# Optimization experiments

Measured on AMD Instinct MI355X. Metric: run time of the kernel, lower is better.

Reference implementation:

```python
import jax, jax.numpy as jnp
import numpy as np

N_TAU = 10      # hardcoded in source (dt = tau / N_tau)
N_STEPS = 500   # N = floor(T/dt) with T=50, tau=1.0 -> dt=0.1
B, D, H = 1024, 128, 512


def setup_inputs() -> dict:
    key = jax.random.key(0)
    k0, k1, k2 = jax.random.split(key, 3)
    return {
        "x0": jax.random.normal(k0, (B, D), dtype=jnp.float32),
        "tau": jnp.ones((1,), dtype=jnp.float32),
        "W1": jax.random.normal(k1, (H, 2 * D + 1), dtype=jnp.float32) * (2 * D + 1) ** -0.5,
        "b1": jnp.zeros((H,), dtype=jnp.float32),
        "W2": jax.random.normal(k2, (D, H), dtype=jnp.float32) * H ** -0.5,
        "b2": jnp.zeros((D,), dtype=jnp.float32),
    }


def reference(x0, tau, W1, b1, W2, b2):
    """Forward-Euler DDE solve: x'(t) = F(x(t), x(t-tau), t), x(t)=x0 for t<=0.
    F(x, y, t) = W2 @ tanh(W1 @ [x; y; t] + b1) + b2, batched over B trajectories.
    Returns the trajectory with shape [N_STEPS+1, B, D]."""
    dt = tau[0] / N_TAU

    def F(x, y, t):
        # x, y: [B, D]; t: traced scalar
        tcol = jnp.full((x.shape[0], 1), 1.0, x.dtype) * t
        z = jnp.concatenate([x, y, tcol], axis=-1)          # [B, 2D+1]
        h = jnp.tanh(z @ W1.T + b1)                          # [B, H]
        return h @ W2.T + b2                                 # [B, D]

    # delay buffer: buf[0] = x_{n-N_tau} (delayed state), buf[-1] = x_n (current)
    buf0 = jnp.broadcast_to(x0, (N_TAU + 1,) + x0.shape)     # constant history X0

    def step(buf, n):
        t = n.astype(x0.dtype) * dt
        x_new = buf[-1] + dt * F(buf[-1], buf[0], t)
        buf = jnp.concatenate([buf[1:], x_new[None]], axis=0)
        return buf, x_new

    _, xs = jax.lax.scan(step, buf0, jnp.arange(N_STEPS))
    return jnp.concatenate([x0[None], xs], axis=0)           # [N+1, B, D]
```

## Files before the change

### kernel.cpp

```cpp
#include <hip/hip_runtime.h>

typedef float f32x4 __attribute__((ext_vector_type(4)));
typedef _Float16 f16x8 __attribute__((ext_vector_type(8)));

#define B_TOT   1024
#define D_DIM   128
#define H_DIM   512
#define N_STEPS 500
#define ROWS    4
#define WAVES   8

#define HSTRIDE 272
#define HSLOT   (8 * HSTRIDE)
#define BSTRIDE 1056
#define LDS_BOUNCE (11 * HSLOT)
#define LDS_TOTAL  (LDS_BOUNCE + 8 * BSTRIDE)

static __device__ __forceinline__ short f16b(float f) {
    _Float16 h = (_Float16)f;
    return __builtin_bit_cast(short, h);
}
static __device__ __forceinline__ float f16tof(short s) {
    return (float)__builtin_bit_cast(_Float16, s);
}
static __device__ __forceinline__ float tanh_fast(float x) {
    float e = __builtin_amdgcn_exp2f(x * 2.885390081777927f);
    return 1.0f - 2.0f * __builtin_amdgcn_rcpf(e + 1.0f);
}
static __device__ __forceinline__ f32x4 sx32(f32x4 v) {
    f32x4 r;
#pragma unroll
    for (int i = 0; i < 4; ++i) r[i] = __shfl_xor(v[i], 32);
    return r;
}
static __device__ __forceinline__ float pick(f32x4 v, int g) {
    float lo = (g & 1) ? v[1] : v[0];
    float hi = (g & 1) ? v[3] : v[2];
    return (g & 2) ? hi : lo;
}

__global__ __launch_bounds__(512, 2) void ndde_kernel(
    const float* __restrict__ x0, const float* __restrict__ tau,
    const float* __restrict__ W1, const float* __restrict__ b1,
    const float* __restrict__ W2, const float* __restrict__ b2,
    float* __restrict__ out)
{
    __shared__ __align__(16) char smem[LDS_TOTAL];

    const int tid = threadIdx.x;
    const int w   = tid >> 6;
    const int l   = tid & 63;
    const int g   = l >> 4;
    const int l15 = l & 15;
    const int ur  = (l15 & 3) | ((l15 >> 3) << 2);
    const int r0  = blockIdx.x * ROWS;
    const int d   = 16 * w + l15;

    const float dtv = tau[0] * 0.1f;

    f16x8 w1f[4][8];
    f16x8 w2f[16];
    float b1f[4], w1tf[4];

#pragma unroll
    for (int nt = 0; nt < 4; ++nt) {
        const int hr = 64 * w + 16 * nt + l15;
        const float* wr = W1 + (long)hr * 257;
#pragma unroll
        for (int ks = 0; ks < 8; ++ks) {
            const int c0 = 32 * ks + 8 * g;
            f16x8 f;
#pragma unroll
            for (int j = 0; j < 8; ++j) f[j] = (_Float16)wr[c0 + j];
            w1f[nt][ks] = f;
        }
        b1f[nt]  = b1[hr];
        w1tf[nt] = wr[256];
    }
    {
        const float* wr = W2 + (long)d * 512;
#pragma unroll
        for (int ks = 0; ks < 16; ++ks) {
            const int c0 = 32 * ks + 8 * g;
            f16x8 f;
#pragma unroll
            for (int j = 0; j < 8; ++j) f[j] = (_Float16)wr[c0 + j];
            w2f[ks] = f;
        }
    }
    const float b2v = b2[d];
    float xo = x0[(long)(r0 + g) * D_DIM + d];

    {
        short hb = f16b(xo);
        short lb = f16b(xo - f16tof(hb));
        for (int s = 0; s < 11; ++s) {
            *(short*)(smem + s * HSLOT + g * HSTRIDE + 2 * d)       = hb;
            *(short*)(smem + s * HSLOT + (g + 4) * HSTRIDE + 2 * d) = lb;
        }
        out[(long)(r0 + g) * D_DIM + d] = xo;
    }
    __syncthreads();

    const int histRd   = ur * HSTRIDE + 16 * g;
    const int bounceRd = LDS_BOUNCE + ur * BSTRIDE + ((16 * g) ^ ((ur & 3) << 4));
    const int bwXor    = g << 4;

    float* po = out + (long)(B_TOT * D_DIM) + (long)(r0 + g) * D_DIM + d;

    int cur = 0;
    int ys  = 1;

#pragma clang loop unroll(disable)
    for (int n = 0; n < N_STEPS; ++n) {
        const float t = (float)n * dtv;

        f32x4 acc1[4];
#pragma unroll
        for (int nt = 0; nt < 4; ++nt) acc1[nt] = (f32x4){0.f, 0.f, 0.f, 0.f};

        const char* xb = smem + cur * HSLOT + histRd;
        const char* yb = smem + ys * HSLOT + histRd;
#pragma unroll
        for (int ks = 0; ks < 4; ++ks) {
            f16x8 xa = *(const f16x8*)(xb + 64 * ks);
#pragma unroll
            for (int nt = 0; nt < 4; ++nt)
                acc1[nt] = __builtin_amdgcn_mfma_f32_16x16x32_f16(xa, w1f[nt][ks], acc1[nt], 0, 0, 0);
        }
#pragma unroll
        for (int ks = 0; ks < 4; ++ks) {
            f16x8 ya = *(const f16x8*)(yb + 64 * ks);
#pragma unroll
            for (int nt = 0; nt < 4; ++nt)
                acc1[nt] = __builtin_amdgcn_mfma_f32_16x16x32_f16(ya, w1f[nt][ks + 4], acc1[nt], 0, 0, 0);
        }

#pragma unroll
        for (int nt = 0; nt < 4; ++nt) {
            f32x4 c = acc1[nt];
            c += sx32(c);
            float hp = pick(c, g) + fmaf(t, w1tf[nt], b1f[nt]);
            float h  = tanh_fast(hp);
            short hh = f16b(h);
            short hl = f16b(h - f16tof(hh));
            const int cb = (2 * (64 * w + 16 * nt + l15)) ^ bwXor;
            *(short*)(smem + LDS_BOUNCE + g * BSTRIDE + cb)       = hh;
            *(short*)(smem + LDS_BOUNCE + (g + 4) * BSTRIDE + cb) = hl;
        }
        __syncthreads();

        f32x4 acc2 = (f32x4){0.f, 0.f, 0.f, 0.f};
#pragma unroll
        for (int ks = 0; ks < 16; ++ks) {
            f16x8 ha = *(const f16x8*)(smem + bounceRd + 64 * ks);
            acc2 = __builtin_amdgcn_mfma_f32_16x16x32_f16(ha, w2f[ks], acc2, 0, 0, 0);
        }
        acc2 += sx32(acc2);

        const float o  = pick(acc2, g) + b2v;
        const float xn = fmaf(dtv, o, xo);
        xo = xn;
        {
            short hb = f16b(xn);
            short lb = f16b(xn - f16tof(hb));
            *(short*)(smem + ys * HSLOT + g * HSTRIDE + 2 * d)       = hb;
            *(short*)(smem + ys * HSLOT + (g + 4) * HSTRIDE + 2 * d) = lb;
        }
        *po = xn;
        po += B_TOT * D_DIM;

        cur = ys;
        ys  = ys + 1;
        if (ys == 11) ys = 0;
        __syncthreads();
    }
}

extern "C" void kernel_launch(void* const* d_in, const int* in_sizes, int n_in,
                              void* d_out, int out_size, void* d_ws, size_t ws_size,
                              hipStream_t stream) {
    (void)in_sizes; (void)n_in; (void)out_size; (void)d_ws; (void)ws_size;
    const float* x0  = (const float*)d_in[0];
    const float* tau = (const float*)d_in[1];
    const float* W1  = (const float*)d_in[2];
    const float* b1  = (const float*)d_in[3];
    const float* W2  = (const float*)d_in[4];
    const float* b2  = (const float*)d_in[5];
    float* out = (float*)d_out;

    ndde_kernel<<<dim3(B_TOT / ROWS), dim3(64 * WAVES), 0, stream>>>(
        x0, tau, W1, b1, W2, b2, out);
}
```

Before: 948.1 us.

## Keep layer-2 inputs in registers, split W2 by hidden slice, reduce partials across waves

Each wave now computes the first layer transposed (weights as the A operand), so the tanh activations stay in registers as the B operand of second-layer MFMAs over that wave's own 64-row hidden slice. Partial D outputs are written to an LDS slab and summed across the 8 waves by a scalar reduction. This removes the activation bounce through LDS. The bias and time term are folded into an extra small MFMA, and the half-wave reduction now uses a DPP lane swap instead of shuffles. In exchange it issues twice as many second-layer MFMAs (hi and lo parts of the activation) and adds an 8-way cross-wave LDS reduction.

```diff
diff --git a/kernel.cpp b/kernel.cpp
--- a/kernel.cpp
+++ b/kernel.cpp
@@ -2,41 +2,31 @@
 
 typedef float f32x4 __attribute__((ext_vector_type(4)));
 typedef _Float16 f16x8 __attribute__((ext_vector_type(8)));
+typedef _Float16 f16x4 __attribute__((ext_vector_type(4)));
+typedef int i32x4 __attribute__((ext_vector_type(4)));
+typedef int i32x2 __attribute__((ext_vector_type(2)));
 
 #define B_TOT   1024
 #define D_DIM   128
-#define H_DIM   512
 #define N_STEPS 500
 #define ROWS    4
 #define WAVES   8
 
 #define HSTRIDE 272
 #define HSLOT   (8 * HSTRIDE)
-#define BSTRIDE 1056
-#define LDS_BOUNCE (11 * HSLOT)
-#define LDS_TOTAL  (LDS_BOUNCE + 8 * BSTRIDE)
-
-static __device__ __forceinline__ short f16b(float f) {
-    _Float16 h = (_Float16)f;
-    return __builtin_bit_cast(short, h);
-}
-static __device__ __forceinline__ float f16tof(short s) {
-    return (float)__builtin_bit_cast(_Float16, s);
-}
+#define SLAB    (11 * HSLOT)
+#define SWSTR   2112
+#define SBSTR   528
+#define LDSSZ   (SLAB + WAVES * SWSTR)
+
 static __device__ __forceinline__ float tanh_fast(float x) {
     float e = __builtin_amdgcn_exp2f(x * 2.885390081777927f);
     return 1.0f - 2.0f * __builtin_amdgcn_rcpf(e + 1.0f);
 }
-static __device__ __forceinline__ f32x4 sx32(f32x4 v) {
-    f32x4 r;
-#pragma unroll
-    for (int i = 0; i < 4; ++i) r[i] = __shfl_xor(v[i], 32);
-    return r;
-}
-static __device__ __forceinline__ float pick(f32x4 v, int g) {
-    float lo = (g & 1) ? v[1] : v[0];
-    float hi = (g & 1) ? v[3] : v[2];
-    return (g & 2) ? hi : lo;
+static __device__ __forceinline__ float xor8_add(float x) {
+    int xi = __builtin_bit_cast(int, x);
+    int yi = __builtin_amdgcn_update_dpp(xi, xi, 0x128, 0xF, 0xF, false);
+    return x + __builtin_bit_cast(float, yi);
 }
 
 __global__ __launch_bounds__(512, 2) void ndde_kernel(
@@ -45,22 +35,25 @@
     const float* __restrict__ W2, const float* __restrict__ b2,
     float* __restrict__ out)
 {
-    __shared__ __align__(16) char smem[LDS_TOTAL];
+    __shared__ __align__(16) char smem[LDSSZ];
 
     const int tid = threadIdx.x;
     const int w   = tid >> 6;
     const int l   = tid & 63;
     const int g   = l >> 4;
     const int l15 = l & 15;
-    const int ur  = (l15 & 3) | ((l15 >> 3) << 2);
+    const int b_l = l15 & 3;
+    const int ur  = b_l + 4 * (l15 >> 3);
+    const int msel = l15 >> 2;
     const int r0  = blockIdx.x * ROWS;
-    const int d   = 16 * w + l15;
+    const int rb  = tid >> 7;
+    const int rd  = tid & 127;
 
     const float dtv = tau[0] * 0.1f;
 
-    f16x8 w1f[4][8];
-    f16x8 w2f[16];
-    float b1f[4], w1tf[4];
+    i32x4 w1s[4][8];
+    i32x2 w2s[8][4];
+    i32x2 wbs[4];
 
 #pragma unroll
     for (int nt = 0; nt < 4; ++nt) {
@@ -72,41 +65,57 @@
             f16x8 f;
 #pragma unroll
             for (int j = 0; j < 8; ++j) f[j] = (_Float16)wr[c0 + j];
-            w1f[nt][ks] = f;
-        }
-        b1f[nt]  = b1[hr];
-        w1tf[nt] = wr[256];
-    }
+            w1s[nt][ks] = __builtin_bit_cast(i32x4, f);
+        }
+        float wt = wr[256];
+        _Float16 wh = (_Float16)wt;
+        _Float16 wl = (_Float16)(wt - (float)wh);
+        f16x4 ab = (g == 0) ? (f16x4){wh, wl, wh, (_Float16)b1[hr]}
+                            : (f16x4){(_Float16)0.f, (_Float16)0.f, (_Float16)0.f, (_Float16)0.f};
+        wbs[nt] = __builtin_bit_cast(i32x2, ab);
+    }
+#pragma unroll
+    for (int mt = 0; mt < 8; ++mt) {
+        const float* wr = W2 + (long)(16 * mt + l15) * 512;
+#pragma unroll
+        for (int s = 0; s < 4; ++s) {
+            const int c0 = 64 * w + 16 * s + 4 * g;
+            f16x4 f;
+#pragma unroll
+            for (int j = 0; j < 4; ++j) f[j] = (_Float16)wr[c0 + j];
+            w2s[mt][s] = __builtin_bit_cast(i32x2, f);
+        }
+    }
+#pragma unroll
+    for (int nt = 0; nt < 4; ++nt) {
+#pragma unroll
+        for (int ks = 0; ks < 8; ++ks) asm volatile("" : "+v"(w1s[nt][ks]));
+        asm volatile("" : "+v"(wbs[nt]));
+    }
+#pragma unroll
+    for (int mt = 0; mt < 8; ++mt)
+#pragma unroll
+        for (int s = 0; s < 4; ++s) asm volatile("" : "+v"(w2s[mt][s]));
+
+    const float b2v = b2[rd];
+    float xo = x0[(long)(r0 + rb) * D_DIM + rd];
+
     {
-        const float* wr = W2 + (long)d * 512;
-#pragma unroll
-        for (int ks = 0; ks < 16; ++ks) {
-            const int c0 = 32 * ks + 8 * g;
-            f16x8 f;
-#pragma unroll
-            for (int j = 0; j < 8; ++j) f[j] = (_Float16)wr[c0 + j];
-            w2f[ks] = f;
-        }
-    }
-    const float b2v = b2[d];
-    float xo = x0[(long)(r0 + g) * D_DIM + d];
-
-    {
-        short hb = f16b(xo);
-        short lb = f16b(xo - f16tof(hb));
+        _Float16 hh = (_Float16)xo;
+        _Float16 hl = (_Float16)(xo - (float)hh);
         for (int s = 0; s < 11; ++s) {
-            *(short*)(smem + s * HSLOT + g * HSTRIDE + 2 * d)       = hb;
-            *(short*)(smem + s * HSLOT + (g + 4) * HSTRIDE + 2 * d) = lb;
-        }
-        out[(long)(r0 + g) * D_DIM + d] = xo;
+            *(short*)(smem + s * HSLOT + rb * HSTRIDE + 2 * rd)               = __builtin_bit_cast(short, hh);
+            *(short*)(smem + s * HSLOT + (rb + 4) * HSTRIDE + 2 * rd)         = __builtin_bit_cast(short, hl);
+        }
+        out[(long)(r0 + rb) * D_DIM + rd] = xo;
     }
     __syncthreads();
 
-    const int histRd   = ur * HSTRIDE + 16 * g;
-    const int bounceRd = LDS_BOUNCE + ur * BSTRIDE + ((16 * g) ^ ((ur & 3) << 4));
-    const int bwXor    = g << 4;
-
-    float* po = out + (long)(B_TOT * D_DIM) + (long)(r0 + g) * D_DIM + d;
+    const int histRd  = ur * HSTRIDE + 16 * g;
+    const int slabWr  = SLAB + w * SWSTR + b_l * SBSTR + 64 * msel + 16 * g;
+    const int slabRd  = SLAB + rb * SBSTR + 4 * rd;
+    const int histWr  = rb * HSTRIDE + 2 * rd;
+    const long outIdx = (long)(r0 + rb) * D_DIM + rd;
 
     int cur = 0;
     int ys  = 1;
@@ -114,10 +123,17 @@
 #pragma clang loop unroll(disable)
     for (int n = 0; n < N_STEPS; ++n) {
         const float t = (float)n * dtv;
+        _Float16 th = (_Float16)t;
+        _Float16 tl = (_Float16)(t - (float)th);
+        f16x4 bt = (g == 0 && l15 < 8)
+                 ? (f16x4){th, th, tl, (_Float16)1.f}
+                 : (f16x4){(_Float16)0.f, (_Float16)0.f, (_Float16)0.f, (_Float16)0.f};
 
         f32x4 acc1[4];
 #pragma unroll
-        for (int nt = 0; nt < 4; ++nt) acc1[nt] = (f32x4){0.f, 0.f, 0.f, 0.f};
+        for (int nt = 0; nt < 4; ++nt)
+            acc1[nt] = __builtin_amdgcn_mfma_f32_16x16x16f16(
+                __builtin_bit_cast(f16x4, wbs[nt]), bt, (f32x4){0.f, 0.f, 0.f, 0.f}, 0, 0, 0);
 
         const char* xb = smem + cur * HSLOT + histRd;
         const char* yb = smem + ys * HSLOT + histRd;
@@ -126,53 +142,70 @@
             f16x8 xa = *(const f16x8*)(xb + 64 * ks);
 #pragma unroll
             for (int nt = 0; nt < 4; ++nt)
-                acc1[nt] = __builtin_amdgcn_mfma_f32_16x16x32_f16(xa, w1f[nt][ks], acc1[nt], 0, 0, 0);
+                acc1[nt] = __builtin_amdgcn_mfma_f32_16x16x32_f16(
+                    __builtin_bit_cast(f16x8, w1s[nt][ks]), xa, acc1[nt], 0, 0, 0);
         }
 #pragma unroll
         for (int ks = 0; ks < 4; ++ks) {
             f16x8 ya = *(const f16x8*)(yb + 64 * ks);
 #pragma unroll
             for (int nt = 0; nt < 4; ++nt)
-                acc1[nt] = __builtin_amdgcn_mfma_f32_16x16x32_f16(ya, w1f[nt][ks + 4], acc1[nt], 0, 0, 0);
-        }
-
-#pragma unroll
-        for (int nt = 0; nt < 4; ++nt) {
-            f32x4 c = acc1[nt];
-            c += sx32(c);
-            float hp = pick(c, g) + fmaf(t, w1tf[nt], b1f[nt]);
-            float h  = tanh_fast(hp);
-            short hh = f16b(h);
-            short hl = f16b(h - f16tof(hh));
-            const int cb = (2 * (64 * w + 16 * nt + l15)) ^ bwXor;
-            *(short*)(smem + LDS_BOUNCE + g * BSTRIDE + cb)       = hh;
-            *(short*)(smem + LDS_BOUNCE + (g + 4) * BSTRIDE + cb) = hl;
+                acc1[nt] = __builtin_amdgcn_mfma_f32_16x16x32_f16(
+                    __builtin_bit_cast(f16x8, w1s[nt][ks + 4]), ya, acc1[nt], 0, 0, 0);
+        }
+
+        f16x4 pbh[4], pbl[4];
+#pragma unroll
+        for (int s = 0; s < 4; ++s) {
+#pragma unroll
+            for (int r = 0; r < 4; ++r) {
+                float v = xor8_add(acc1[s][r]);
+                float h = tanh_fast(v);
+                _Float16 hh = (_Float16)h;
+                pbh[s][r] = hh;
+                pbl[s][r] = (_Float16)(h - (float)hh);
+            }
+        }
+
+#pragma unroll
+        for (int half = 0; half < 2; ++half) {
+            f32x4 a2[4];
+#pragma unroll
+            for (int m = 0; m < 4; ++m) a2[m] = (f32x4){0.f, 0.f, 0.f, 0.f};
+#pragma unroll
+            for (int s = 0; s < 4; ++s) {
+#pragma unroll
+                for (int m = 0; m < 4; ++m) {
+                    const int mt = 4 * half + m;
+                    a2[m] = __builtin_amdgcn_mfma_f32_16x16x16f16(
+                        __builtin_bit_cast(f16x4, w2s[mt][s]), pbh[s], a2[m], 0, 0, 0);
+                    a2[m] = __builtin_amdgcn_mfma_f32_16x16x16f16(
+                        __builtin_bit_cast(f16x4, w2s[mt][s]), pbl[s], a2[m], 0, 0, 0);
+                }
+            }
+            f32x4 v01 = (msel & 1) ? a2[1] : a2[0];
+            f32x4 v23 = (msel & 1) ? a2[3] : a2[2];
+            f32x4 vw  = (msel & 2) ? v23 : v01;
+            *(f32x4*)(smem + slabWr + half * 256) = vw;
         }
         __syncthreads();
 
-        f32x4 acc2 = (f32x4){0.f, 0.f, 0.f, 0.f};
-#pragma unroll
-        for (int ks = 0; ks < 16; ++ks) {
-            f16x8 ha = *(const f16x8*)(smem + bounceRd + 64 * ks);
-            acc2 = __builtin_amdgcn_mfma_f32_16x16x32_f16(ha, w2f[ks], acc2, 0, 0, 0);
-        }
-        acc2 += sx32(acc2);
-
-        const float o  = pick(acc2, g) + b2v;
-        const float xn = fmaf(dtv, o, xo);
+        float acc = 0.f;
+#pragma unroll
+        for (int wv = 0; wv < 8; ++wv)
+            acc += *(const float*)(smem + slabRd + wv * SWSTR);
+        const float xn = fmaf(dtv, acc + b2v, xo);
         xo = xn;
         {
-            short hb = f16b(xn);
-            short lb = f16b(xn - f16tof(hb));
-            *(short*)(smem + ys * HSLOT + g * HSTRIDE + 2 * d)       = hb;
-            *(short*)(smem + ys * HSLOT + (g + 4) * HSTRIDE + 2 * d) = lb;
-        }
-        *po = xn;
-        po += B_TOT * D_DIM;
+            _Float16 hh = (_Float16)xn;
+            _Float16 hl = (_Float16)(xn - (float)hh);
+            *(short*)(smem + ys * HSLOT + histWr)               = __builtin_bit_cast(short, hh);
+            *(short*)(smem + ys * HSLOT + 4 * HSTRIDE + histWr) = __builtin_bit_cast(short, hl);
+        }
+        out[outIdx + (long)(n + 1) * (B_TOT * D_DIM)] = xn;
 
         cur = ys;
-        ys  = ys + 1;
-        if (ys == 11) ys = 0;
+        ys  = (ys == 10) ? 0 : ys + 1;
         __syncthreads();
     }
 }
```

Result: slower. 1.221 ms (+28.8%).

## Precompute next step's delayed-state GEMM during layer-2 and split accumulator chains

Applied to the files above, without the earlier changes.

Moves the delayed-input half of the first-layer MFMA (which does not depend on the current step's result) off the critical path. It is now computed for the next step right after the layer-2 MFMAs, so the serial chain per step holds only the x-half. Layer 2 is split into four independent accumulator chains that are summed at the end, shortening MFMA dependency latency. __syncthreads is replaced by an explicit lgkmcnt wait plus s_barrier. This raises register pressure, and the reassociated f32 sums change rounding slightly.

```diff
diff --git a/kernel.cpp b/kernel.cpp
--- a/kernel.cpp
+++ b/kernel.cpp
@@ -37,6 +37,10 @@
     float lo = (g & 1) ? v[1] : v[0];
     float hi = (g & 1) ? v[3] : v[2];
     return (g & 2) ? hi : lo;
+}
+static __device__ __forceinline__ void barrier_lds() {
+    asm volatile("s_waitcnt lgkmcnt(0)" ::: "memory");
+    __builtin_amdgcn_s_barrier();
 }
 
 __global__ __launch_bounds__(512, 2) void ndde_kernel(
@@ -111,34 +115,36 @@
     int cur = 0;
     int ys  = 1;
 
+    f32x4 accY[4];
+#pragma unroll
+    for (int nt = 0; nt < 4; ++nt) accY[nt] = (f32x4){0.f, 0.f, 0.f, 0.f};
+    {
+        const char* yb = smem + 1 * HSLOT + histRd;
+#pragma unroll
+        for (int ks = 0; ks < 4; ++ks) {
+            f16x8 ya = *(const f16x8*)(yb + 64 * ks);
+#pragma unroll
+            for (int nt = 0; nt < 4; ++nt)
+                accY[nt] = __builtin_amdgcn_mfma_f32_16x16x32_f16(ya, w1f[nt][ks + 4], accY[nt], 0, 0, 0);
+        }
+    }
+
 #pragma clang loop unroll(disable)
     for (int n = 0; n < N_STEPS; ++n) {
         const float t = (float)n * dtv;
 
-        f32x4 acc1[4];
-#pragma unroll
-        for (int nt = 0; nt < 4; ++nt) acc1[nt] = (f32x4){0.f, 0.f, 0.f, 0.f};
-
         const char* xb = smem + cur * HSLOT + histRd;
-        const char* yb = smem + ys * HSLOT + histRd;
 #pragma unroll
         for (int ks = 0; ks < 4; ++ks) {
             f16x8 xa = *(const f16x8*)(xb + 64 * ks);
 #pragma unroll
             for (int nt = 0; nt < 4; ++nt)
-                acc1[nt] = __builtin_amdgcn_mfma_f32_16x16x32_f16(xa, w1f[nt][ks], acc1[nt], 0, 0, 0);
-        }
-#pragma unroll
-        for (int ks = 0; ks < 4; ++ks) {
-            f16x8 ya = *(const f16x8*)(yb + 64 * ks);
-#pragma unroll
-            for (int nt = 0; nt < 4; ++nt)
-                acc1[nt] = __builtin_amdgcn_mfma_f32_16x16x32_f16(ya, w1f[nt][ks + 4], acc1[nt], 0, 0, 0);
+                accY[nt] = __builtin_amdgcn_mfma_f32_16x16x32_f16(xa, w1f[nt][ks], accY[nt], 0, 0, 0);
         }
 
 #pragma unroll
         for (int nt = 0; nt < 4; ++nt) {
-            f32x4 c = acc1[nt];
+            f32x4 c = accY[nt];
             c += sx32(c);
             float hp = pick(c, g) + fmaf(t, w1tf[nt], b1f[nt]);
             float h  = tanh_fast(hp);
@@ -148,16 +154,35 @@
             *(short*)(smem + LDS_BOUNCE + g * BSTRIDE + cb)       = hh;
             *(short*)(smem + LDS_BOUNCE + (g + 4) * BSTRIDE + cb) = hl;
         }
-        __syncthreads();
-
-        f32x4 acc2 = (f32x4){0.f, 0.f, 0.f, 0.f};
-#pragma unroll
-        for (int ks = 0; ks < 16; ++ks) {
-            f16x8 ha = *(const f16x8*)(smem + bounceRd + 64 * ks);
-            acc2 = __builtin_amdgcn_mfma_f32_16x16x32_f16(ha, w2f[ks], acc2, 0, 0, 0);
-        }
+        barrier_lds();
+
+        f32x4 a2c[4];
+#pragma unroll
+        for (int c = 0; c < 4; ++c) {
+            a2c[c] = (f32x4){0.f, 0.f, 0.f, 0.f};
+#pragma unroll
+            for (int k = 0; k < 4; ++k) {
+                f16x8 ha = *(const f16x8*)(smem + bounceRd + 64 * (4 * c + k));
+                a2c[c] = __builtin_amdgcn_mfma_f32_16x16x32_f16(ha, w2f[4 * c + k], a2c[c], 0, 0, 0);
+            }
+        }
+
+        const int ysN = (ys == 10) ? 0 : ys + 1;
+#pragma unroll
+        for (int nt = 0; nt < 4; ++nt) accY[nt] = (f32x4){0.f, 0.f, 0.f, 0.f};
+        {
+            const char* yb = smem + ysN * HSLOT + histRd;
+#pragma unroll
+            for (int ks = 0; ks < 4; ++ks) {
+                f16x8 ya = *(const f16x8*)(yb + 64 * ks);
+#pragma unroll
+                for (int nt = 0; nt < 4; ++nt)
+                    accY[nt] = __builtin_amdgcn_mfma_f32_16x16x32_f16(ya, w1f[nt][ks + 4], accY[nt], 0, 0, 0);
+            }
+        }
+
+        f32x4 acc2 = (a2c[0] + a2c[1]) + (a2c[2] + a2c[3]);
         acc2 += sx32(acc2);
-
         const float o  = pick(acc2, g) + b2v;
         const float xn = fmaf(dtv, o, xo);
         xo = xn;
@@ -171,9 +196,8 @@
         po += B_TOT * D_DIM;
 
         cur = ys;
-        ys  = ys + 1;
-        if (ys == 11) ys = 0;
-        __syncthreads();
+        ys  = ysN;
+        barrier_lds();
     }
 }
 
```

After: 991.2 us, median of 2. +4.5%, slower.
